# Optimization experiments

Hardware: AMD Instinct MI355X
Metric: run time of the kernel (lower is better)

The kernel has to match this reference:

```python
import jax, jax.numpy as jnp
import numpy as np


def setup_inputs() -> dict:
    key = jax.random.key(0)
    k1, k2 = jax.random.split(key)
    B, D, T = 16, 128, 4096
    K = 1024
    z = jax.random.normal(k1, (B, D, T), dtype=jnp.float32)
    # codebook initialized ~ kaiming uniform in the original; randn is fine as a stand-in
    codebook = jax.random.normal(k2, (K, D), dtype=jnp.float32)
    return {"z": z, "codebook": codebook}


def reference(z, codebook):
    # z: [B, D, T], codebook: [K, D]
    B, D, T = z.shape
    # encode: flatten to tokens [B*T, D] (matches z.permute(0,2,1).reshape(-1, D))
    flat_z = jnp.transpose(z, (0, 2, 1)).reshape(-1, D)
    d2 = (
        jnp.sum(flat_z * flat_z, axis=1, keepdims=True)
        - 2.0 * (flat_z @ codebook.T)
        + jnp.sum(codebook * codebook, axis=1)[None, :]
    )
    indices = jnp.argmin(d2, axis=1)  # [B*T]
    # decode: embedding gather, reshape back to [B, D, T]
    quantized = codebook[indices]  # [B*T, D]
    return jnp.transpose(quantized.reshape(B, T, D), (0, 2, 1))
```

## Files before the change

### kernel.cpp

```cpp
#include <hip/hip_runtime.h>


#define Dd 128
#define Tt 4096
#define Kc 1024
#define DT (Dd*Tt)
#define DELTA 0.3f
#define NEG_INF (-__builtin_inff())

typedef float  floatx4 __attribute__((ext_vector_type(4)));
typedef short  shortx8 __attribute__((ext_vector_type(8)));

__device__ __forceinline__ unsigned f2bf(float f) {
  unsigned u = __float_as_uint(f);
  u = u + 0x7fffu + ((u >> 16) & 1u);
  return u >> 16;
}

#define ASYNC_COPY16(dst, src) \
  __builtin_amdgcn_global_load_lds((const __attribute__((address_space(1))) void*)(src), \
                                   (__attribute__((address_space(3))) void*)(dst), 16, 0, 0)

__global__ __launch_bounds__(256) void vq_prep(const float* __restrict__ cb,
                                               unsigned short* __restrict__ cbbf,
                                               float* __restrict__ bias,
                                               double* __restrict__ cc64) {
  int c = blockIdx.x * 256 + threadIdx.x;
  if (c >= Kc) return;
  const float4* row = (const float4*)(cb + (size_t)c * Dd);
  uint2* dst = (uint2*)(cbbf + (size_t)c * Dd);
  double s = 0.0;
  #pragma unroll 8
  for (int q = 0; q < 32; q++) {
    float4 v = row[q];
    s = fma((double)v.x, (double)v.x, s);
    s = fma((double)v.y, (double)v.y, s);
    s = fma((double)v.z, (double)v.z, s);
    s = fma((double)v.w, (double)v.w, s);
    uint2 p;
    p.x = f2bf(v.x) | (f2bf(v.y) << 16);
    p.y = f2bf(v.z) | (f2bf(v.w) << 16);
    dst[q] = p;
  }
  cc64[c] = s;
  bias[c] = (float)(-0.5 * s);
}

__global__ __launch_bounds__(256, 2) void vq_stage1(const float* __restrict__ z,
                                                    const float* __restrict__ cb,
                                                    const unsigned short* __restrict__ cbbf,
                                                    const float* __restrict__ bias,
                                                    unsigned* __restrict__ counter,
                                                    unsigned* __restrict__ list,
                                                    float* __restrict__ out) {
  __shared__ uint4 cb_lds4[2048];
  __shared__ uint4 z_lds4[2048];
  __shared__ float2 res[128][8];
  __shared__ unsigned idxlds[128];
  char* cb_lds = (char*)cb_lds4;
  char* z_lds  = (char*)z_lds4;

  const int tid  = threadIdx.x;
  const int lane = tid & 63;
  const int wid  = tid >> 6;
  const int wm   = wid & 1;
  const int wn   = wid >> 1;
  const int lrow = lane >> 4;
  const int lcol = lane & 15;

  const int token0 = blockIdx.x * 128;
  const int b  = token0 >> 12;
  const int t0 = token0 & 4095;

  {
    const int token = tid & 127;
    const int dh = tid >> 7;
    const float* zb = z + (size_t)b * DT + (size_t)(t0 + token);
    #pragma unroll 4
    for (int i = 0; i < 32; i++) {
      int d = (i * 2 + dh) * 2;
      float f0 = zb[(size_t)d * Tt];
      float f1 = zb[(size_t)(d + 1) * Tt];
      unsigned u = f2bf(f0) | (f2bf(f1) << 16);
      unsigned off = ((unsigned)(token * 256 + d * 2)) ^ (((unsigned)(token & 7)) << 4);
      *(unsigned*)(z_lds + off) = u;
    }
  }

  float M1[4], M2[4];
  #pragma unroll
  for (int nf = 0; nf < 4; nf++) { M1[nf] = NEG_INF; M2[nf] = NEG_INF; }

  #pragma unroll 1
  for (int cc = 0; cc < 8; cc++) {
    const int ccbase = cc * 128;
    __syncthreads();
    #pragma unroll
    for (int i = 0; i < 8; i++) {
      unsigned db  = (unsigned)(i * 4096 + wid * 1024 + lane * 16);
      unsigned row = db >> 8;
      unsigned kb  = db & 255u;
      const char* src = (const char*)cbbf + (((unsigned)ccbase + row) << 8) + (kb ^ ((row & 7u) << 4));
      char* dst = cb_lds + i * 4096 + wid * 1024;
      ASYNC_COPY16(dst, src);
    }
    floatx4 acc[4][4];
    #pragma unroll
    for (int mf = 0; mf < 4; mf++) {
      floatx4 bv = *(const floatx4*)(bias + ccbase + wm * 64 + mf * 16 + lrow * 4);
      #pragma unroll
      for (int nf = 0; nf < 4; nf++) acc[mf][nf] = bv;
    }
    __syncthreads();

    #pragma unroll
    for (int ks = 0; ks < 4; ks++) {
      shortx8 af[4], bfr[4];
      const int kbyte = (ks * 32 + lrow * 8) * 2;
      #pragma unroll
      for (int mf = 0; mf < 4; mf++) {
        int row = wm * 64 + mf * 16 + lcol;
        af[mf] = *(const shortx8*)(cb_lds + (((unsigned)(row * 256 + kbyte)) ^ (((unsigned)(row & 7)) << 4)));
      }
      #pragma unroll
      for (int nf = 0; nf < 4; nf++) {
        int row = wn * 64 + nf * 16 + lcol;
        bfr[nf] = *(const shortx8*)(z_lds + (((unsigned)(row * 256 + kbyte)) ^ (((unsigned)(row & 7)) << 4)));
      }
      #pragma unroll
      for (int mf = 0; mf < 4; mf++)
        #pragma unroll
        for (int nf = 0; nf < 4; nf++)
          acc[mf][nf] = __builtin_amdgcn_mfma_f32_16x16x32_bf16(af[mf], bfr[nf], acc[mf][nf], 0, 0, 0);
    }

    #pragma unroll
    for (int mf = 0; mf < 4; mf++) {
      const unsigned ib = (unsigned)(ccbase + wm * 64 + mf * 16 + lrow * 4);
      #pragma unroll
      for (int j = 0; j < 4; j++) {
        const unsigned idx = ib + j;
        #pragma unroll
        for (int nf = 0; nf < 4; nf++) {
          float s  = acc[mf][nf][j];
          float pf = __uint_as_float((__float_as_uint(s) & 0xFFFFFC00u) | idx);
          float tm = fminf(pf, M1[nf]);
          M2[nf] = fmaxf(M2[nf], tm);
          M1[nf] = fmaxf(M1[nf], pf);
        }
      }
    }
  }

  #pragma unroll
  for (int nf = 0; nf < 4; nf++) {
    int token = wn * 64 + nf * 16 + lcol;
    res[token][wm * 4 + lrow] = make_float2(M1[nf], M2[nf]);
  }
  __syncthreads();

  if (tid < 128) {
    float g1 = NEG_INF, g2 = NEG_INF;
    #pragma unroll
    for (int s = 0; s < 8; s++) {
      float2 v = res[tid][s];
      float tm = fminf(v.x, g1);
      g1 = fmaxf(g1, v.x);
      g2 = fmaxf(g2, tm);
      g2 = fmaxf(g2, v.y);
    }
    unsigned idx = __float_as_uint(g1) & 1023u;
    idxlds[tid] = idx;
    if (g1 - g2 < DELTA) {
      unsigned pos = atomicAdd(counter, 1u);
      list[pos] = (unsigned)(token0 + tid);
    }
  }
  __syncthreads();

  {
    const int token = tid & 127;
    const int half  = tid >> 7;
    const unsigned idx = idxlds[token];
    const float4* crow = (const float4*)(cb + (size_t)idx * Dd);
    const size_t obase = (size_t)b * DT + (size_t)(t0 + token);
    #pragma unroll
    for (int q = 0; q < 16; q++) {
      int d = half * 64 + q * 4;
      float4 v = crow[d >> 2];
      out[obase + (size_t)(d + 0) * Tt] = v.x;
      out[obase + (size_t)(d + 1) * Tt] = v.y;
      out[obase + (size_t)(d + 2) * Tt] = v.z;
      out[obase + (size_t)(d + 3) * Tt] = v.w;
    }
  }
}

__global__ __launch_bounds__(256) void vq_rescue(const float* __restrict__ z,
                                                 const float* __restrict__ cb,
                                                 const double* __restrict__ cc64,
                                                 const unsigned* __restrict__ counter,
                                                 const unsigned* __restrict__ list,
                                                 float* __restrict__ out) {
  const int tid = threadIdx.x;
  const unsigned count = *counter;
  __shared__ float zbuf[8][128];
  __shared__ double zz[8];
  __shared__ double rv[4][8];
  __shared__ int    rc[4][8];
  __shared__ int    fidx[8];
  __shared__ unsigned toks[8];

  for (unsigned base = blockIdx.x * 8u; base < count; base += gridDim.x * 8u) {
    unsigned rem = count - base;
    int nt = rem < 8u ? (int)rem : 8;
    __syncthreads();
    if (tid < nt) toks[tid] = list[base + tid];
    __syncthreads();
    for (int e = tid; e < nt * 128; e += 256) {
      int j = e >> 7, d = e & 127;
      unsigned tk = toks[j];
      zbuf[j][d] = z[(size_t)(tk >> 12) * DT + (size_t)d * Tt + (tk & 4095u)];
    }
    __syncthreads();
    if (tid < 8) {
      double s = 0.0;
      #pragma unroll 16
      for (int d = 0; d < 128; d++) {
        double v = (double)zbuf[tid][d];
        s = fma(v, v, s);
      }
      zz[tid] = s;
    }

    double acc[8][4];
    #pragma unroll
    for (int j = 0; j < 8; j++)
      #pragma unroll
      for (int q = 0; q < 4; q++) acc[j][q] = 0.0;

    for (int d0 = 0; d0 < 128; d0 += 4) {
      double cvd[4][4];
      #pragma unroll
      for (int q = 0; q < 4; q++) {
        float4 cv = *(const float4*)(cb + (size_t)(q * 256 + tid) * Dd + d0);
        cvd[q][0] = (double)cv.x; cvd[q][1] = (double)cv.y;
        cvd[q][2] = (double)cv.z; cvd[q][3] = (double)cv.w;
      }
      #pragma unroll
      for (int j = 0; j < 8; j++) {
        float4 zv = *(const float4*)&zbuf[j][d0];
        double z0 = (double)zv.x, z1 = (double)zv.y, z2 = (double)zv.z, z3 = (double)zv.w;
        #pragma unroll
        for (int q = 0; q < 4; q++)
          acc[j][q] = fma(z0, cvd[q][0], fma(z1, cvd[q][1], fma(z2, cvd[q][2], fma(z3, cvd[q][3], acc[j][q]))));
      }
    }
    __syncthreads();

    #pragma unroll
    for (int j = 0; j < 8; j++) {
      double bv = __builtin_inf(); int bc = 0x7fffffff;
      double zzj = zz[j];
      #pragma unroll
      for (int q = 0; q < 4; q++) {
        int c = q * 256 + tid;
        double d2 = zzj - 2.0 * acc[j][q] + cc64[c];
        if (d2 < bv || (d2 == bv && c < bc)) { bv = d2; bc = c; }
      }
      #pragma unroll
      for (int off = 32; off > 0; off >>= 1) {
        double ov = __shfl_xor(bv, off);
        int    oc = __shfl_xor(bc, off);
        if (ov < bv || (ov == bv && oc < bc)) { bv = ov; bc = oc; }
      }
      if ((tid & 63) == 0) { rv[tid >> 6][j] = bv; rc[tid >> 6][j] = bc; }
    }
    __syncthreads();
    if (tid < 8) {
      int j = tid; double bv = rv[0][j]; int bc = rc[0][j];
      #pragma unroll
      for (int w = 1; w < 4; w++) {
        double ov = rv[w][j]; int oc = rc[w][j];
        if (ov < bv || (ov == bv && oc < bc)) { bv = ov; bc = oc; }
      }
      fidx[j] = bc;
    }
    __syncthreads();
    for (int j = 0; j < nt; j++) {
      unsigned tk = toks[j];
      int c = fidx[j];
      for (int d = tid; d < 128; d += 256)
        out[(size_t)(tk >> 12) * DT + (size_t)d * Tt + (tk & 4095u)] = cb[(size_t)c * Dd + d];
    }
  }
}

extern "C" void kernel_launch(void* const* d_in, const int* in_sizes, int n_in,
                              void* d_out, int out_size, void* d_ws, size_t ws_size,
                              hipStream_t stream) {
  const float* z  = (const float*)d_in[0];
  const float* cb = (const float*)d_in[1];
  float* out = (float*)d_out;

  char* ws = (char*)d_ws;
  unsigned*       counter = (unsigned*)ws;
  float*          bias    = (float*)(ws + (4u << 10));
  double*         cc64    = (double*)(ws + (16u << 10));
  unsigned short* cbbf    = (unsigned short*)(ws + (32u << 10));
  unsigned*       list    = (unsigned*)(ws + (288u << 10));

  hipMemsetAsync(d_ws, 0, 4, stream);
  hipLaunchKernelGGL(vq_prep,   dim3(4),   dim3(256), 0, stream, cb, cbbf, bias, cc64);
  hipLaunchKernelGGL(vq_stage1, dim3(512), dim3(256), 0, stream, z, cb, cbbf, bias, counter, list, out);
  hipLaunchKernelGGL(vq_rescue, dim3(512), dim3(256), 0, stream, z, cb, cc64, counter, list, out);
}
```

Baseline: 241.9 us.

## Use split-bf16 triple MFMA for near-fp32 distances and shrink rescue margin

Splits both the codebook and z tiles into bf16 high and low parts and accumulates three MFMAs per fragment (hh, lh, hl), giving roughly fp32-accurate dot products. This lets the ambiguity margin for the fp64 rescue pass drop from 0.3 to 0.005, so far fewer tokens reach the slow rescue kernel. The argmin index is now tracked explicitly instead of being packed into the low mantissa bits, and flagged tokens are first batched in LDS and then appended with a single global atomic per block. In exchange stage1 does three times the MFMA work, doubles LDS (about 64KB of tiles, with the occupancy hint of 2 removed) and doubles codebook traffic per block.

```diff
diff --git a/kernel.cpp b/kernel.cpp
--- a/kernel.cpp
+++ b/kernel.cpp
@@ -5,7 +5,7 @@
 #define Tt 4096
 #define Kc 1024
 #define DT (Dd*Tt)
-#define DELTA 0.3f
+#define DELTA 0.005f
 #define NEG_INF (-__builtin_inff())
 
 typedef float  floatx4 __attribute__((ext_vector_type(4)));
@@ -16,19 +16,22 @@
   u = u + 0x7fffu + ((u >> 16) & 1u);
   return u >> 16;
 }
+__device__ __forceinline__ float bf2f(unsigned h) { return __uint_as_float(h << 16); }
 
 #define ASYNC_COPY16(dst, src) \
   __builtin_amdgcn_global_load_lds((const __attribute__((address_space(1))) void*)(src), \
                                    (__attribute__((address_space(3))) void*)(dst), 16, 0, 0)
 
 __global__ __launch_bounds__(256) void vq_prep(const float* __restrict__ cb,
-                                               unsigned short* __restrict__ cbbf,
+                                               unsigned short* __restrict__ cbh,
+                                               unsigned short* __restrict__ cbl,
                                                float* __restrict__ bias,
                                                double* __restrict__ cc64) {
   int c = blockIdx.x * 256 + threadIdx.x;
   if (c >= Kc) return;
   const float4* row = (const float4*)(cb + (size_t)c * Dd);
-  uint2* dst = (uint2*)(cbbf + (size_t)c * Dd);
+  uint2* dh = (uint2*)(cbh + (size_t)c * Dd);
+  uint2* dl = (uint2*)(cbl + (size_t)c * Dd);
   double s = 0.0;
   #pragma unroll 8
   for (int q = 0; q < 32; q++) {
@@ -37,28 +40,35 @@
     s = fma((double)v.y, (double)v.y, s);
     s = fma((double)v.z, (double)v.z, s);
     s = fma((double)v.w, (double)v.w, s);
-    uint2 p;
-    p.x = f2bf(v.x) | (f2bf(v.y) << 16);
-    p.y = f2bf(v.z) | (f2bf(v.w) << 16);
-    dst[q] = p;
+    unsigned h0 = f2bf(v.x), h1 = f2bf(v.y), h2 = f2bf(v.z), h3 = f2bf(v.w);
+    unsigned l0 = f2bf(v.x - bf2f(h0)), l1 = f2bf(v.y - bf2f(h1));
+    unsigned l2 = f2bf(v.z - bf2f(h2)), l3 = f2bf(v.w - bf2f(h3));
+    uint2 ph; ph.x = h0 | (h1 << 16); ph.y = h2 | (h3 << 16);
+    uint2 pl; pl.x = l0 | (l1 << 16); pl.y = l2 | (l3 << 16);
+    dh[q] = ph; dl[q] = pl;
   }
   cc64[c] = s;
   bias[c] = (float)(-0.5 * s);
 }
 
-__global__ __launch_bounds__(256, 2) void vq_stage1(const float* __restrict__ z,
-                                                    const float* __restrict__ cb,
-                                                    const unsigned short* __restrict__ cbbf,
-                                                    const float* __restrict__ bias,
-                                                    unsigned* __restrict__ counter,
-                                                    unsigned* __restrict__ list,
-                                                    float* __restrict__ out) {
-  __shared__ uint4 cb_lds4[2048];
-  __shared__ uint4 z_lds4[2048];
-  __shared__ float2 res[128][8];
+__global__ __launch_bounds__(256) void vq_stage1(const float* __restrict__ z,
+                                                 const float* __restrict__ cb,
+                                                 const unsigned short* __restrict__ cbh,
+                                                 const unsigned short* __restrict__ cbl,
+                                                 const float* __restrict__ bias,
+                                                 unsigned* __restrict__ counter,
+                                                 unsigned* __restrict__ list,
+                                                 float* __restrict__ out) {
+  __shared__ uint4 zh4[2048];
+  __shared__ uint4 zl4[2048];
+  __shared__ uint4 ch4[2048];
+  __shared__ uint4 cl4[2048];
+  __shared__ float4 res[128][8];
   __shared__ unsigned idxlds[128];
-  char* cb_lds = (char*)cb_lds4;
-  char* z_lds  = (char*)z_lds4;
+  __shared__ unsigned flg_list[128];
+  __shared__ unsigned flg_n, flg_base;
+  char* zh_lds = (char*)zh4; char* zl_lds = (char*)zl4;
+  char* ch_lds = (char*)ch4; char* cl_lds = (char*)cl4;
 
   const int tid  = threadIdx.x;
   const int lane = tid & 63;
@@ -72,24 +82,29 @@
   const int b  = token0 >> 12;
   const int t0 = token0 & 4095;
 
+  if (tid == 0) flg_n = 0;
+
   {
     const int token = tid & 127;
-    const int dh = tid >> 7;
+    const int dhalf = tid >> 7;
     const float* zb = z + (size_t)b * DT + (size_t)(t0 + token);
     #pragma unroll 4
     for (int i = 0; i < 32; i++) {
-      int d = (i * 2 + dh) * 2;
+      int d = (i * 2 + dhalf) * 2;
       float f0 = zb[(size_t)d * Tt];
       float f1 = zb[(size_t)(d + 1) * Tt];
-      unsigned u = f2bf(f0) | (f2bf(f1) << 16);
+      unsigned h0 = f2bf(f0), h1 = f2bf(f1);
+      unsigned l0 = f2bf(f0 - bf2f(h0)), l1 = f2bf(f1 - bf2f(h1));
       unsigned off = ((unsigned)(token * 256 + d * 2)) ^ (((unsigned)(token & 7)) << 4);
-      *(unsigned*)(z_lds + off) = u;
+      *(unsigned*)(zh_lds + off) = h0 | (h1 << 16);
+      *(unsigned*)(zl_lds + off) = l0 | (l1 << 16);
     }
   }
 
   float M1[4], M2[4];
+  unsigned I1[4];
   #pragma unroll
-  for (int nf = 0; nf < 4; nf++) { M1[nf] = NEG_INF; M2[nf] = NEG_INF; }
+  for (int nf = 0; nf < 4; nf++) { M1[nf] = NEG_INF; M2[nf] = NEG_INF; I1[nf] = 0; }
 
   #pragma unroll 1
   for (int cc = 0; cc < 8; cc++) {
@@ -100,9 +115,9 @@
       unsigned db  = (unsigned)(i * 4096 + wid * 1024 + lane * 16);
       unsigned row = db >> 8;
       unsigned kb  = db & 255u;
-      const char* src = (const char*)cbbf + (((unsigned)ccbase + row) << 8) + (kb ^ ((row & 7u) << 4));
-      char* dst = cb_lds + i * 4096 + wid * 1024;
-      ASYNC_COPY16(dst, src);
+      unsigned goff = (((unsigned)ccbase + row) << 8) + (kb ^ ((row & 7u) << 4));
+      ASYNC_COPY16(ch_lds + i * 4096 + wid * 1024, (const char*)cbh + goff);
+      ASYNC_COPY16(cl_lds + i * 4096 + wid * 1024, (const char*)cbl + goff);
     }
     floatx4 acc[4][4];
     #pragma unroll
@@ -115,23 +130,30 @@
 
     #pragma unroll
     for (int ks = 0; ks < 4; ks++) {
-      shortx8 af[4], bfr[4];
+      shortx8 ah[4], al[4], bh[4], bl[4];
       const int kbyte = (ks * 32 + lrow * 8) * 2;
       #pragma unroll
       for (int mf = 0; mf < 4; mf++) {
         int row = wm * 64 + mf * 16 + lcol;
-        af[mf] = *(const shortx8*)(cb_lds + (((unsigned)(row * 256 + kbyte)) ^ (((unsigned)(row & 7)) << 4)));
+        unsigned off = ((unsigned)(row * 256 + kbyte)) ^ (((unsigned)(row & 7)) << 4);
+        ah[mf] = *(const shortx8*)(ch_lds + off);
+        al[mf] = *(const shortx8*)(cl_lds + off);
       }
       #pragma unroll
       for (int nf = 0; nf < 4; nf++) {
         int row = wn * 64 + nf * 16 + lcol;
-        bfr[nf] = *(const shortx8*)(z_lds + (((unsigned)(row * 256 + kbyte)) ^ (((unsigned)(row & 7)) << 4)));
+        unsigned off = ((unsigned)(row * 256 + kbyte)) ^ (((unsigned)(row & 7)) << 4);
+        bh[nf] = *(const shortx8*)(zh_lds + off);
+        bl[nf] = *(const shortx8*)(zl_lds + off);
       }
       #pragma unroll
       for (int mf = 0; mf < 4; mf++)
         #pragma unroll
-        for (int nf = 0; nf < 4; nf++)
-          acc[mf][nf] = __builtin_amdgcn_mfma_f32_16x16x32_bf16(af[mf], bfr[nf], acc[mf][nf], 0, 0, 0);
+        for (int nf = 0; nf < 4; nf++) {
+          acc[mf][nf] = __builtin_amdgcn_mfma_f32_16x16x32_bf16(ah[mf], bh[nf], acc[mf][nf], 0, 0, 0);
+          acc[mf][nf] = __builtin_amdgcn_mfma_f32_16x16x32_bf16(al[mf], bh[nf], acc[mf][nf], 0, 0, 0);
+          acc[mf][nf] = __builtin_amdgcn_mfma_f32_16x16x32_bf16(ah[mf], bl[nf], acc[mf][nf], 0, 0, 0);
+        }
     }
 
     #pragma unroll
@@ -142,11 +164,11 @@
         const unsigned idx = ib + j;
         #pragma unroll
         for (int nf = 0; nf < 4; nf++) {
-          float s  = acc[mf][nf][j];
-          float pf = __uint_as_float((__float_as_uint(s) & 0xFFFFFC00u) | idx);
-          float tm = fminf(pf, M1[nf]);
-          M2[nf] = fmaxf(M2[nf], tm);
-          M1[nf] = fmaxf(M1[nf], pf);
+          float s = acc[mf][nf][j];
+          bool gt = s > M1[nf];
+          M2[nf] = fmaxf(M2[nf], fminf(s, M1[nf]));
+          I1[nf] = gt ? idx : I1[nf];
+          M1[nf] = fmaxf(M1[nf], s);
         }
       }
     }
@@ -155,28 +177,31 @@
   #pragma unroll
   for (int nf = 0; nf < 4; nf++) {
     int token = wn * 64 + nf * 16 + lcol;
-    res[token][wm * 4 + lrow] = make_float2(M1[nf], M2[nf]);
+    res[token][wm * 4 + lrow] = make_float4(M1[nf], M2[nf], __uint_as_float(I1[nf]), 0.f);
   }
   __syncthreads();
 
   if (tid < 128) {
-    float g1 = NEG_INF, g2 = NEG_INF;
+    float g1 = NEG_INF, g2 = NEG_INF; unsigned gi = 0;
     #pragma unroll
     for (int s = 0; s < 8; s++) {
-      float2 v = res[tid][s];
-      float tm = fminf(v.x, g1);
+      float4 v = res[tid][s];
+      bool better = v.x > g1;
+      float loser = better ? g1 : v.x;
+      g2 = fmaxf(g2, fmaxf(loser, v.y));
+      gi = better ? __float_as_uint(v.z) : gi;
       g1 = fmaxf(g1, v.x);
-      g2 = fmaxf(g2, tm);
-      g2 = fmaxf(g2, v.y);
-    }
-    unsigned idx = __float_as_uint(g1) & 1023u;
-    idxlds[tid] = idx;
+    }
+    idxlds[tid] = gi;
     if (g1 - g2 < DELTA) {
-      unsigned pos = atomicAdd(counter, 1u);
-      list[pos] = (unsigned)(token0 + tid);
+      unsigned p = atomicAdd(&flg_n, 1u);
+      flg_list[p] = (unsigned)(token0 + tid);
     }
   }
   __syncthreads();
+  if (tid == 0 && flg_n > 0) flg_base = atomicAdd(counter, flg_n);
+  __syncthreads();
+  if (tid < flg_n) list[flg_base + tid] = flg_list[tid];
 
   {
     const int token = tid & 127;
@@ -307,11 +332,12 @@
   unsigned*       counter = (unsigned*)ws;
   float*          bias    = (float*)(ws + (4u << 10));
   double*         cc64    = (double*)(ws + (16u << 10));
-  unsigned short* cbbf    = (unsigned short*)(ws + (32u << 10));
-  unsigned*       list    = (unsigned*)(ws + (288u << 10));
+  unsigned short* cbh     = (unsigned short*)(ws + (32u << 10));
+  unsigned short* cbl     = (unsigned short*)(ws + (288u << 10));
+  unsigned*       list    = (unsigned*)(ws + (544u << 10));
 
   hipMemsetAsync(d_ws, 0, 4, stream);
-  hipLaunchKernelGGL(vq_prep,   dim3(4),   dim3(256), 0, stream, cb, cbbf, bias, cc64);
-  hipLaunchKernelGGL(vq_stage1, dim3(512), dim3(256), 0, stream, z, cb, cbbf, bias, counter, list, out);
+  hipLaunchKernelGGL(vq_prep,   dim3(4),   dim3(256), 0, stream, cb, cbh, cbl, bias, cc64);
+  hipLaunchKernelGGL(vq_stage1, dim3(512), dim3(256), 0, stream, z, cb, cbh, cbl, bias, counter, list, out);
   hipLaunchKernelGGL(vq_rescue, dim3(512), dim3(256), 0, stream, z, cb, cc64, counter, list, out);
 }
```

Result: faster. 208.7 us (-13.7%).
